# Optimization experiments

Hardware: AMD Instinct MI355X
Metric: run time of the kernel (lower is better)

## Reference

```python
import jax, jax.numpy as jnp
import numpy as np

B, S, D = 2, 2048, 2048
H, KVH, HD = 16, 4, 128
GROUPS = H // KVH
SCALE = HD ** -0.5


def rotate_half(x):
    half = x.shape[-1] // 2
    return jnp.concatenate((-x[..., half:], x[..., :half]), axis=-1)


def apply_rope(q, k, cos, sin):
    # q,k: [B,S,H,HD]; cos,sin: [S,HD//2] -> repeat_interleave(2) -> [S,HD]
    cos = jnp.repeat(cos, 2, axis=-1)[None, :, None, :]
    sin = jnp.repeat(sin, 2, axis=-1)[None, :, None, :]
    return q * cos + rotate_half(q) * sin, k * cos + rotate_half(k) * sin


def setup_inputs() -> dict:
    key = jax.random.key(0)
    ks = jax.random.split(key, 8)
    inp = {
        'x': jax.random.normal(ks[0], (B, S, D), dtype=jnp.float32),
        'cos': jnp.cos(jnp.arange(S, dtype=jnp.float32)[:, None] * (1.0 / (10000.0 ** (jnp.arange(HD // 2, dtype=jnp.float32) / (HD // 2))))[None, :].reshape(1, HD // 2)),
        'sin': None,
        'mask': jnp.tril(jnp.ones((S, S), dtype=bool))[None, None, :, :],
        'Wq': jax.random.normal(ks[1], (D, H * HD), dtype=jnp.float32) * (D ** -0.5),
        'Wk': jax.random.normal(ks[2], (D, KVH * HD), dtype=jnp.float32) * (D ** -0.5),
        'Wv': jax.random.normal(ks[3], (D, KVH * HD), dtype=jnp.float32) * (D ** -0.5),
        'Wo': jax.random.normal(ks[4], (H * HD, D), dtype=jnp.float32) * ((H * HD) ** -0.5),
    }
    inv_freq = 1.0 / (10000.0 ** (jnp.arange(0, HD // 2, dtype=jnp.float32) / (HD // 2)))
    freqs = jnp.arange(S, dtype=jnp.float32)[:, None] * inv_freq[None, :]  # [S, HD//2]
    inp['cos'] = jnp.cos(freqs)
    inp['sin'] = jnp.sin(freqs)
    return inp


def reference(x, cos, sin, mask, Wq, Wk, Wv, Wo):
    b, s, _ = x.shape
    q = (x @ Wq).reshape(b, s, H, HD)    # [B,S,H,HD]
    k = (x @ Wk).reshape(b, s, KVH, HD)  # [B,S,KVH,HD]
    v = (x @ Wv).reshape(b, s, KVH, HD)
    q, k = apply_rope(q, k, cos, sin)
    q = q.transpose(0, 2, 1, 3)  # [B,H,S,HD]
    k = k.transpose(0, 2, 1, 3)  # [B,KVH,S,HD]
    v = v.transpose(0, 2, 1, 3)
    k = jnp.repeat(k, GROUPS, axis=1)  # [B,H,S,HD]
    v = jnp.repeat(v, GROUPS, axis=1)
    scores = jnp.einsum('bhqd,bhkd->bhqk', q, k) * SCALE
    scores = jnp.where(mask, scores, -jnp.inf)
    attn = jax.nn.softmax(scores, axis=-1)
    out = jnp.einsum('bhqk,bhkd->bhqd', attn, v)
    out = out.transpose(0, 2, 1, 3).reshape(b, s, H * HD)
    return out @ Wo
```

## Files before the change

kernel.cpp:

```cpp
#include <hip/hip_runtime.h>
#include <hip/hip_bf16.h>
#include <cstdint>
#include <type_traits>

typedef __attribute__((ext_vector_type(8))) short short8;
typedef __attribute__((ext_vector_type(4))) float floatx4;

constexpr int S_LEN = 2048;
constexpr float ATTN_SCALE = 0.08838834764831845f;
constexpr float LOG2E = 1.4426950408889634f;
constexpr float CP = ATTN_SCALE * LOG2E;

__device__ __forceinline__ void gl_lds16(const void* gp, void* lp) {
  __builtin_amdgcn_global_load_lds(
      (__attribute__((address_space(1))) void*)(uintptr_t)gp,
      (__attribute__((address_space(3))) void*)lp,
      16, 0, 0);
}

__device__ __forceinline__ float rowmax16(float x) {
  union { float f; int i; } a, b;
  a.f = x;
  b.i = __builtin_amdgcn_update_dpp(0, a.i, 0x121, 0xF, 0xF, true);
  x = fmaxf(x, b.f); a.f = x;
  b.i = __builtin_amdgcn_update_dpp(0, a.i, 0x122, 0xF, 0xF, true);
  x = fmaxf(x, b.f); a.f = x;
  b.i = __builtin_amdgcn_update_dpp(0, a.i, 0x124, 0xF, 0xF, true);
  x = fmaxf(x, b.f); a.f = x;
  b.i = __builtin_amdgcn_update_dpp(0, a.i, 0x128, 0xF, 0xF, true);
  return fmaxf(x, b.f);
}

__global__ void cvt_bf16_kernel(const float* __restrict__ src,
                                __hip_bfloat16* __restrict__ dst, int n4) {
  int i = blockIdx.x * blockDim.x + threadIdx.x;
  if (i >= n4) return;
  float4 f = reinterpret_cast<const float4*>(src)[i];
  union { unsigned long long u64; __hip_bfloat16 h[4]; } u;
  u.h[0] = __float2bfloat16(f.x);
  u.h[1] = __float2bfloat16(f.y);
  u.h[2] = __float2bfloat16(f.z);
  u.h[3] = __float2bfloat16(f.w);
  reinterpret_cast<unsigned long long*>(dst)[i] = u.u64;
}

__global__ void transpose_bf16_kernel(const float* __restrict__ src,
                                      __hip_bfloat16* __restrict__ dst,
                                      int K, int N) {
  __shared__ float tile[32][33];
  int n0 = blockIdx.x * 32, k0 = blockIdx.y * 32;
  int tx = threadIdx.x, ty = threadIdx.y;
#pragma unroll
  for (int i = ty; i < 32; i += 8)
    tile[i][tx] = src[(size_t)(k0 + i) * N + n0 + tx];
  __syncthreads();
#pragma unroll
  for (int i = ty; i < 32; i += 8)
    dst[(size_t)(n0 + i) * K + k0 + tx] = __float2bfloat16(tile[tx][i]);
}

__global__ __launch_bounds__(256, 2) void qkv_gemm_kernel(
    const __hip_bfloat16* __restrict__ A,
    const __hip_bfloat16* __restrict__ Bt,
    __hip_bfloat16* __restrict__ qbuf,
    __hip_bfloat16* __restrict__ kbuf,
    __hip_bfloat16* __restrict__ vbuf) {
  constexpr int K = 2048;
  __shared__ __align__(16) __hip_bfloat16 lds[2 * 128 * 64];
  const int tid = threadIdx.x;
  const int wave = tid >> 6, lane = tid & 63;
  const int quad = lane >> 4, l15 = lane & 15;
  const int wm = wave >> 1, wn = wave & 1;
  const int m0 = blockIdx.y * 128, n0 = blockIdx.x * 128;

  floatx4 acc[4][4] = {};
  const __hip_bfloat16* Ab = A + (size_t)m0 * K;
  const __hip_bfloat16* Bb = Bt + (size_t)n0 * K;
  const int i0 = wave * 4;

  for (int k0 = 0; k0 < K; k0 += 64) {
#pragma unroll
    for (int j = 0; j < 4; ++j) {
      const int i = i0 + j;
      const int kchunk = i >> 1;
      const int row = ((i & 1) << 6) | lane;
      gl_lds16(Ab + (size_t)row * K + (k0 + kchunk * 8), &lds[i * 512]);
      gl_lds16(Bb + (size_t)row * K + (k0 + kchunk * 8), &lds[8192 + i * 512]);
    }
    __syncthreads();
#pragma unroll
    for (int kk = 0; kk < 2; ++kk) {
      short8 a[4], b[4];
#pragma unroll
      for (int mi = 0; mi < 4; ++mi)
        a[mi] = *(const short8*)&lds[((((kk << 2) | quad) * 128) + wm * 64 + mi * 16 + l15) * 8];
#pragma unroll
      for (int ni = 0; ni < 4; ++ni)
        b[ni] = *(const short8*)&lds[8192 + ((((kk << 2) | quad) * 128) + wn * 64 + ni * 16 + l15) * 8];
#pragma unroll
      for (int mi = 0; mi < 4; ++mi)
#pragma unroll
        for (int ni = 0; ni < 4; ++ni)
          acc[mi][ni] = __builtin_amdgcn_mfma_f32_16x16x32_bf16(a[mi], b[ni], acc[mi][ni], 0, 0, 0);
    }
    __syncthreads();
  }

  const int region = (n0 - 2048) >> 7;
  const int kvh = region & 3;
#pragma unroll
  for (int mi = 0; mi < 4; ++mi)
#pragma unroll
    for (int ni = 0; ni < 4; ++ni)
#pragma unroll
      for (int r = 0; r < 4; ++r) {
        int row = m0 + wm * 64 + mi * 16 + quad * 4 + r;
        int col = n0 + wn * 64 + ni * 16 + l15;
        __hip_bfloat16 val = __float2bfloat16(acc[mi][ni][r]);
        if (n0 < 2048) {
          qbuf[(size_t)row * 2048 + col] = val;
        } else {
          int d = wn * 64 + ni * 16 + l15;
          int s = row & (S_LEN - 1), bb = row >> 11;
          size_t tb = ((size_t)(bb * 4 + kvh) * 32 + (s >> 6)) * 8192;
          int kv = s & 63;
          if (region < 4)
            kbuf[tb + ((d >> 3) << 9) + (kv << 3) + (d & 7)] = val;
          else
            vbuf[tb + d * 64 + (kv ^ ((d & 7) << 3))] = val;
        }
      }
}

__global__ __launch_bounds__(256, 2) void gemm_bt_f32_kernel(
    const __hip_bfloat16* __restrict__ A,
    const __hip_bfloat16* __restrict__ Bt,
    float* __restrict__ C, int N, int K) {
  __shared__ __align__(16) __hip_bfloat16 lds[2 * 128 * 64];
  const int tid = threadIdx.x;
  const int wave = tid >> 6, lane = tid & 63;
  const int quad = lane >> 4, l15 = lane & 15;
  const int wm = wave >> 1, wn = wave & 1;
  const int m0 = blockIdx.y * 128, n0 = blockIdx.x * 128;

  floatx4 acc[4][4] = {};
  const __hip_bfloat16* Ab = A + (size_t)m0 * K;
  const __hip_bfloat16* Bb = Bt + (size_t)n0 * K;
  const int i0 = wave * 4;

  for (int k0 = 0; k0 < K; k0 += 64) {
#pragma unroll
    for (int j = 0; j < 4; ++j) {
      const int i = i0 + j;
      const int kchunk = i >> 1;
      const int row = ((i & 1) << 6) | lane;
      gl_lds16(Ab + (size_t)row * K + (k0 + kchunk * 8), &lds[i * 512]);
      gl_lds16(Bb + (size_t)row * K + (k0 + kchunk * 8), &lds[8192 + i * 512]);
    }
    __syncthreads();
#pragma unroll
    for (int kk = 0; kk < 2; ++kk) {
      short8 a[4], b[4];
#pragma unroll
      for (int mi = 0; mi < 4; ++mi)
        a[mi] = *(const short8*)&lds[((((kk << 2) | quad) * 128) + wm * 64 + mi * 16 + l15) * 8];
#pragma unroll
      for (int ni = 0; ni < 4; ++ni)
        b[ni] = *(const short8*)&lds[8192 + ((((kk << 2) | quad) * 128) + wn * 64 + ni * 16 + l15) * 8];
#pragma unroll
      for (int mi = 0; mi < 4; ++mi)
#pragma unroll
        for (int ni = 0; ni < 4; ++ni)
          acc[mi][ni] = __builtin_amdgcn_mfma_f32_16x16x32_bf16(a[mi], b[ni], acc[mi][ni], 0, 0, 0);
    }
    __syncthreads();
  }

#pragma unroll
  for (int mi = 0; mi < 4; ++mi)
#pragma unroll
    for (int ni = 0; ni < 4; ++ni)
#pragma unroll
      for (int r = 0; r < 4; ++r) {
        int row = m0 + wm * 64 + mi * 16 + quad * 4 + r;
        int col = n0 + wn * 64 + ni * 16 + l15;
        C[(size_t)row * N + col] = acc[mi][ni][r];
      }
}

__device__ __forceinline__ void rope8(short8 x0, short8 x1, const float* ca,
                                      const float* sa, const float* cb,
                                      const float* sb, short8& y0, short8& y1) {
#pragma unroll
  for (int e = 0; e < 8; ++e) {
    union { short s; __hip_bfloat16 h; } u0, u1, w0, w1;
    u0.s = x0[e]; u1.s = x1[e];
    float f0 = __bfloat162float(u0.h), f1 = __bfloat162float(u1.h);
    int j = e >> 1;
    w0.h = __float2bfloat16(f0 * ca[j] - f1 * sa[j]);
    w1.h = __float2bfloat16(f1 * cb[j] + f0 * sb[j]);
    y0[e] = w0.s; y1[e] = w1.s;
  }
}

__global__ void rope_q_kernel(__hip_bfloat16* __restrict__ qbuf,
                              const float* __restrict__ cosb,
                              const float* __restrict__ sinb) {
  int t = blockIdx.x * blockDim.x + threadIdx.x;
  int c8 = t & 7;
  int head = (t >> 3) & 15;
  int row = t >> 7;
  int s = row & (S_LEN - 1);
  size_t base = (size_t)row * 2048 + head * 128 + c8 * 8;
  short8 x0 = *(const short8*)(qbuf + base);
  short8 x1 = *(const short8*)(qbuf + base + 64);
  float ca[4], sa[4], cb[4], sb[4];
  *(float4*)ca = *(const float4*)&cosb[s * 64 + c8 * 4];
  *(float4*)sa = *(const float4*)&sinb[s * 64 + c8 * 4];
  *(float4*)cb = *(const float4*)&cosb[s * 64 + 32 + c8 * 4];
  *(float4*)sb = *(const float4*)&sinb[s * 64 + 32 + c8 * 4];
  short8 y0, y1;
  rope8(x0, x1, ca, sa, cb, sb, y0, y1);
  *(short8*)(qbuf + base) = y0;
  *(short8*)(qbuf + base + 64) = y1;
}

__global__ void rope_k_kernel(__hip_bfloat16* __restrict__ kbuf,
                              const float* __restrict__ cosb,
                              const float* __restrict__ sinb) {
  int t = blockIdx.x * blockDim.x + threadIdx.x;
  int c8 = t & 7;
  int kv = (t >> 3) & 63;
  int tile = t >> 9;
  int s = (tile & 31) * 64 + kv;
  size_t a0 = (size_t)tile * 8192 + c8 * 512 + kv * 8;
  short8 x0 = *(const short8*)(kbuf + a0);
  short8 x1 = *(const short8*)(kbuf + a0 + 4096);
  float ca[4], sa[4], cb[4], sb[4];
  *(float4*)ca = *(const float4*)&cosb[s * 64 + c8 * 4];
  *(float4*)sa = *(const float4*)&sinb[s * 64 + c8 * 4];
  *(float4*)cb = *(const float4*)&cosb[s * 64 + 32 + c8 * 4];
  *(float4*)sb = *(const float4*)&sinb[s * 64 + 32 + c8 * 4];
  short8 y0, y1;
  rope8(x0, x1, ca, sa, cb, sb, y0, y1);
  *(short8*)(kbuf + a0) = y0;
  *(short8*)(kbuf + a0 + 4096) = y1;
}

__global__ __launch_bounds__(256, 2) void attn_kernel(
    const __hip_bfloat16* __restrict__ qbuf,
    const __hip_bfloat16* __restrict__ kbuf,
    const __hip_bfloat16* __restrict__ vbuf,
    __hip_bfloat16* __restrict__ aout) {
  const int qt = (blockIdx.y & 16) ? blockIdx.x : (15 - blockIdx.x);
  const int bh = blockIdx.y;
  const int b = bh >> 4, h = bh & 15;
  const int kvh = h >> 2;

  __shared__ __align__(16) __hip_bfloat16 Kbuf[2][8192];
  __shared__ __align__(16) __hip_bfloat16 Vbuf[2][8192];
  __shared__ __align__(16) __hip_bfloat16 Plds[4 * 16 * 72];

  const int tid = threadIdx.x;
  const int wave = tid >> 6, lane = tid & 63;
  const int quad = lane >> 4, l15 = lane & 15;

  short8 qfrag[2][4];
#pragma unroll
  for (int rs = 0; rs < 2; ++rs)
#pragma unroll
    for (int kc = 0; kc < 4; ++kc)
      qfrag[rs][kc] = *(const short8*)(qbuf +
          (size_t)(b * S_LEN + qt * 128 + rs * 64 + wave * 16 + l15) * 2048 +
          h * 128 + kc * 32 + quad * 8);

  const __hip_bfloat16* ktiles = kbuf + (size_t)(b * 4 + kvh) * 32 * 8192;
  const __hip_bfloat16* vtiles = vbuf + (size_t)(b * 4 + kvh) * 32 * 8192;
  const int nt = 2 * qt + 2;

#pragma unroll
  for (int j = 0; j < 4; ++j) {
    int c = tid + 256 * j;
    gl_lds16(ktiles + c * 8, &Kbuf[0][c * 8]);
    gl_lds16(vtiles + c * 8, &Vbuf[0][c * 8]);
  }

  float m_r[2][4];
  floatx4 o[2][8] = {};
  floatx4 o_l[2] = {};
#pragma unroll
  for (int rs = 0; rs < 2; ++rs)
#pragma unroll
    for (int r = 0; r < 4; ++r) m_r[rs][r] = -1e30f;

  short8 onesb;
#pragma unroll
  for (int e = 0; e < 8; ++e) onesb[e] = (short)0x3F80;

  __hip_bfloat16* pw = &Plds[wave * 16 * 72];

  for (int kt = 0; kt < nt; ++kt) {
    const int cur = kt & 1;
    __syncthreads();

    if (kt + 1 < nt) {
      const __hip_bfloat16* kb = ktiles + (size_t)(kt + 1) * 8192;
      const __hip_bfloat16* vb = vtiles + (size_t)(kt + 1) * 8192;
#pragma unroll
      for (int j = 0; j < 4; ++j) {
        int c = tid + 256 * j;
        gl_lds16(kb + c * 8, &Kbuf[1 - cur][c * 8]);
        gl_lds16(vb + c * 8, &Vbuf[1 - cur][c * 8]);
      }
    }

    floatx4 sc[2][4] = {};
#pragma unroll
    for (int ni = 0; ni < 4; ++ni)
#pragma unroll
      for (int kc = 0; kc < 4; ++kc) {
        short8 bf = *(const short8*)&Kbuf[cur][((kc * 4 + quad) * 64 + ni * 16 + l15) * 8];
        sc[0][ni] = __builtin_amdgcn_mfma_f32_16x16x32_bf16(qfrag[0][kc], bf, sc[0][ni], 0, 0, 0);
        sc[1][ni] = __builtin_amdgcn_mfma_f32_16x16x32_bf16(qfrag[1][kc], bf, sc[1][ni], 0, 0, 0);
      }

#pragma unroll
    for (int rs = 0; rs < 2; ++rs) {
      const int qt64 = 2 * qt + rs;
      if (kt > qt64) continue;
      if (kt == qt64) {
        const int qrow = qt * 128 + rs * 64 + wave * 16 + quad * 4;
#pragma unroll
        for (int ni = 0; ni < 4; ++ni) {
          int kvcol = kt * 64 + ni * 16 + l15;
#pragma unroll
          for (int r = 0; r < 4; ++r)
            if (kvcol > qrow + r) sc[rs][ni][r] = -1e30f;
        }
      }

      float alpha[4];
#pragma unroll
      for (int r = 0; r < 4; ++r) {
        float v = fmaxf(fmaxf(sc[rs][0][r], sc[rs][1][r]),
                        fmaxf(sc[rs][2][r], sc[rs][3][r]));
        v = rowmax16(v);
        float mnew = fmaxf(m_r[rs][r], v);
        alpha[r] = exp2f((m_r[rs][r] - mnew) * CP);
        m_r[rs][r] = mnew;
        float mc = mnew * CP;
#pragma unroll
        for (int ni = 0; ni < 4; ++ni) {
          float p = exp2f(sc[rs][ni][r] * CP - mc);
          pw[(quad * 4 + r) * 72 + ni * 16 + l15] = __float2bfloat16(p);
        }
      }

#pragma unroll
      for (int nc = 0; nc < 8; ++nc)
#pragma unroll
        for (int r = 0; r < 4; ++r) o[rs][nc][r] *= alpha[r];
#pragma unroll
      for (int r = 0; r < 4; ++r) o_l[rs][r] *= alpha[r];

#pragma unroll
      for (int kk2 = 0; kk2 < 2; ++kk2) {
        short8 pa = *(const short8*)&pw[l15 * 72 + kk2 * 32 + quad * 8];
#pragma unroll
        for (int nc = 0; nc < 8; ++nc) {
          int d = nc * 16 + l15;
          int swcol = (kk2 * 32 + quad * 8) ^ ((d & 7) << 3);
          short8 vv = *(const short8*)&Vbuf[cur][d * 64 + swcol];
          o[rs][nc] = __builtin_amdgcn_mfma_f32_16x16x32_bf16(pa, vv, o[rs][nc], 0, 0, 0);
        }
        o_l[rs] = __builtin_amdgcn_mfma_f32_16x16x32_bf16(pa, onesb, o_l[rs], 0, 0, 0);
      }
    }
  }

#pragma unroll
  for (int rs = 0; rs < 2; ++rs) {
    float inv[4];
#pragma unroll
    for (int r = 0; r < 4; ++r) inv[r] = 1.0f / o_l[rs][r];
    const size_t orow0 = (size_t)(b * S_LEN + qt * 128 + rs * 64 + wave * 16 + quad * 4);
#pragma unroll
    for (int nc = 0; nc < 8; ++nc)
#pragma unroll
      for (int r = 0; r < 4; ++r)
        aout[(orow0 + r) * 2048 + h * 128 + nc * 16 + l15] =
            __float2bfloat16(o[rs][nc][r] * inv[r]);
  }
}

extern "C" void kernel_launch(void* const* d_in, const int* in_sizes, int n_in,
                              void* d_out, int out_size, void* d_ws, size_t ws_size,
                              hipStream_t stream) {
  const float* x    = (const float*)d_in[0];
  const float* cosb = (const float*)d_in[1];
  const float* sinb = (const float*)d_in[2];
  const float* Wq = (const float*)d_in[4];
  const float* Wk = (const float*)d_in[5];
  const float* Wv = (const float*)d_in[6];
  const float* Wo = (const float*)d_in[7];
  float* out = (float*)d_out;

  char* ws = (char*)d_ws;
  __hip_bfloat16* xb    = (__hip_bfloat16*)(ws);
  __hip_bfloat16* wqkvt = (__hip_bfloat16*)(ws + (16u << 20));
  __hip_bfloat16* wot   = (__hip_bfloat16*)(ws + (28u << 20));
  __hip_bfloat16* qbuf  = (__hip_bfloat16*)(ws + (36u << 20));
  __hip_bfloat16* kbuf  = (__hip_bfloat16*)(ws + (52u << 20));
  __hip_bfloat16* vbuf  = (__hip_bfloat16*)(ws + (56u << 20));
  __hip_bfloat16* aout  = (__hip_bfloat16*)(ws + (60u << 20));

  dim3 tb(32, 8);
  cvt_bf16_kernel<<<8192, 256, 0, stream>>>(x, xb, 2097152);
  transpose_bf16_kernel<<<dim3(64, 64), tb, 0, stream>>>(Wq, wqkvt, 2048, 2048);
  transpose_bf16_kernel<<<dim3(16, 64), tb, 0, stream>>>(Wk, wqkvt + 2048 * 2048, 2048, 512);
  transpose_bf16_kernel<<<dim3(16, 64), tb, 0, stream>>>(Wv, wqkvt + 2560 * 2048, 2048, 512);
  transpose_bf16_kernel<<<dim3(64, 64), tb, 0, stream>>>(Wo, wot, 2048, 2048);

  qkv_gemm_kernel<<<dim3(24, 32), 256, 0, stream>>>(xb, wqkvt, qbuf, kbuf, vbuf);
  rope_q_kernel<<<2048, 256, 0, stream>>>(qbuf, cosb, sinb);
  rope_k_kernel<<<512, 256, 0, stream>>>(kbuf, cosb, sinb);
  attn_kernel<<<dim3(16, 32), 256, 0, stream>>>(qbuf, kbuf, vbuf, aout);
  gemm_bt_f32_kernel<<<dim3(16, 32), 256, 0, stream>>>(aout, wot, out, 2048, 2048);
}
```

Measured before the change: 435.1 us.

## Merge prep and rope launches, shrink GEMM tiles to 64x128, batch attention PV MFMAs

Folds the x conversion and four weight transposes into one prep kernel, and merges the q and k rope kernels into one launch, cutting seven launches down to two. Both GEMMs move from 128x128 to 64x128 tiles with occupancy 4, doubling the block count to fill more CUs. The attention inner loop now loads both row-slices' P fragments first, then issues the PV MFMAs for both against each V fragment, so V is read from LDS once. In exchange the GEMMs get less reuse per block, and diagonal tiles now always go through masking.

```diff
diff --git a/kernel.cpp b/kernel.cpp
--- a/kernel.cpp
+++ b/kernel.cpp
@@ -31,90 +31,113 @@
   return fmaxf(x, b.f);
 }
 
-__global__ void cvt_bf16_kernel(const float* __restrict__ src,
-                                __hip_bfloat16* __restrict__ dst, int n4) {
-  int i = blockIdx.x * blockDim.x + threadIdx.x;
-  if (i >= n4) return;
-  float4 f = reinterpret_cast<const float4*>(src)[i];
-  union { unsigned long long u64; __hip_bfloat16 h[4]; } u;
-  u.h[0] = __float2bfloat16(f.x);
-  u.h[1] = __float2bfloat16(f.y);
-  u.h[2] = __float2bfloat16(f.z);
-  u.h[3] = __float2bfloat16(f.w);
-  reinterpret_cast<unsigned long long*>(dst)[i] = u.u64;
-}
-
-__global__ void transpose_bf16_kernel(const float* __restrict__ src,
-                                      __hip_bfloat16* __restrict__ dst,
-                                      int K, int N) {
-  __shared__ float tile[32][33];
-  int n0 = blockIdx.x * 32, k0 = blockIdx.y * 32;
-  int tx = threadIdx.x, ty = threadIdx.y;
+__device__ __forceinline__ void tr32(const float* __restrict__ src,
+                                     __hip_bfloat16* __restrict__ dst,
+                                     int blk, int nblk_x, int N, int tid,
+                                     float (*tile)[33]) {
+  int n0 = (blk % nblk_x) * 32, k0 = (blk / nblk_x) * 32;
+  int tx = tid & 31, ty = tid >> 5;
 #pragma unroll
   for (int i = ty; i < 32; i += 8)
     tile[i][tx] = src[(size_t)(k0 + i) * N + n0 + tx];
   __syncthreads();
 #pragma unroll
   for (int i = ty; i < 32; i += 8)
-    dst[(size_t)(n0 + i) * K + k0 + tx] = __float2bfloat16(tile[tx][i]);
-}
-
-__global__ __launch_bounds__(256, 2) void qkv_gemm_kernel(
+    dst[(size_t)(n0 + i) * 2048 + k0 + tx] = __float2bfloat16(tile[tx][i]);
+}
+
+__global__ void prep_kernel(const float* __restrict__ x,
+                            const float* __restrict__ Wq,
+                            const float* __restrict__ Wk,
+                            const float* __restrict__ Wv,
+                            const float* __restrict__ Wo,
+                            __hip_bfloat16* __restrict__ xb,
+                            __hip_bfloat16* __restrict__ wqkvt,
+                            __hip_bfloat16* __restrict__ wot) {
+  __shared__ float tile[32][33];
+  int bx = blockIdx.x, tid = threadIdx.x;
+  if (bx < 8192) {
+    int i = bx * 256 + tid;
+    float4 f = reinterpret_cast<const float4*>(x)[i];
+    union { unsigned long long u64; __hip_bfloat16 h[4]; } u;
+    u.h[0] = __float2bfloat16(f.x);
+    u.h[1] = __float2bfloat16(f.y);
+    u.h[2] = __float2bfloat16(f.z);
+    u.h[3] = __float2bfloat16(f.w);
+    reinterpret_cast<unsigned long long*>(xb)[i] = u.u64;
+  } else if (bx < 12288) {
+    tr32(Wq, wqkvt, bx - 8192, 64, 2048, tid, tile);
+  } else if (bx < 13312) {
+    tr32(Wk, wqkvt + 2048 * 2048, bx - 12288, 16, 512, tid, tile);
+  } else if (bx < 14336) {
+    tr32(Wv, wqkvt + 2560 * 2048, bx - 13312, 16, 512, tid, tile);
+  } else {
+    tr32(Wo, wot, bx - 14336, 64, 2048, tid, tile);
+  }
+}
+
+#define GEMM_STAGE(Ab, Bb, Alds, Blds, K, k0)                                   \
+  {                                                                             \
+    _Pragma("unroll") for (int j = 0; j < 6; ++j) {                             \
+      const int i = wave * 6 + j;                                               \
+      if (i < 8) {                                                              \
+        gl_lds16(Ab + (size_t)lane * (K) + (k0) + i * 8, &Alds[(i * 64 + lane) * 8]); \
+      } else {                                                                  \
+        const int ii = i - 8, kchunk = ii >> 1, row = ((ii & 1) << 6) | lane;   \
+        gl_lds16(Bb + (size_t)row * (K) + (k0) + kchunk * 8,                    \
+                 &Blds[(kchunk * 128 + row) * 8]);                              \
+      }                                                                         \
+    }                                                                           \
+  }
+
+#define GEMM_COMPUTE(Alds, Blds)                                                \
+  _Pragma("unroll") for (int kk = 0; kk < 2; ++kk) {                            \
+    short8 a[2], b[4];                                                          \
+    _Pragma("unroll") for (int mi = 0; mi < 2; ++mi)                            \
+      a[mi] = *(const short8*)&Alds[(((kk * 4 + quad) * 64) + wm * 32 + mi * 16 + l15) * 8]; \
+    _Pragma("unroll") for (int ni = 0; ni < 4; ++ni)                            \
+      b[ni] = *(const short8*)&Blds[(((kk * 4 + quad) * 128) + wn * 64 + ni * 16 + l15) * 8]; \
+    _Pragma("unroll") for (int mi = 0; mi < 2; ++mi)                            \
+      _Pragma("unroll") for (int ni = 0; ni < 4; ++ni)                          \
+        acc[mi][ni] = __builtin_amdgcn_mfma_f32_16x16x32_bf16(a[mi], b[ni], acc[mi][ni], 0, 0, 0); \
+  }
+
+__global__ __launch_bounds__(256, 4) void qkv_gemm_kernel(
     const __hip_bfloat16* __restrict__ A,
     const __hip_bfloat16* __restrict__ Bt,
     __hip_bfloat16* __restrict__ qbuf,
     __hip_bfloat16* __restrict__ kbuf,
     __hip_bfloat16* __restrict__ vbuf) {
   constexpr int K = 2048;
-  __shared__ __align__(16) __hip_bfloat16 lds[2 * 128 * 64];
+  __shared__ __align__(16) __hip_bfloat16 lds[4096 + 8192];
+  __hip_bfloat16* Alds = lds;
+  __hip_bfloat16* Blds = lds + 4096;
   const int tid = threadIdx.x;
   const int wave = tid >> 6, lane = tid & 63;
   const int quad = lane >> 4, l15 = lane & 15;
   const int wm = wave >> 1, wn = wave & 1;
-  const int m0 = blockIdx.y * 128, n0 = blockIdx.x * 128;
-
-  floatx4 acc[4][4] = {};
+  const int m0 = blockIdx.y * 64, n0 = blockIdx.x * 128;
+
+  floatx4 acc[2][4] = {};
   const __hip_bfloat16* Ab = A + (size_t)m0 * K;
   const __hip_bfloat16* Bb = Bt + (size_t)n0 * K;
-  const int i0 = wave * 4;
 
   for (int k0 = 0; k0 < K; k0 += 64) {
-#pragma unroll
-    for (int j = 0; j < 4; ++j) {
-      const int i = i0 + j;
-      const int kchunk = i >> 1;
-      const int row = ((i & 1) << 6) | lane;
-      gl_lds16(Ab + (size_t)row * K + (k0 + kchunk * 8), &lds[i * 512]);
-      gl_lds16(Bb + (size_t)row * K + (k0 + kchunk * 8), &lds[8192 + i * 512]);
-    }
+    GEMM_STAGE(Ab, Bb, Alds, Blds, K, k0)
     __syncthreads();
-#pragma unroll
-    for (int kk = 0; kk < 2; ++kk) {
-      short8 a[4], b[4];
-#pragma unroll
-      for (int mi = 0; mi < 4; ++mi)
-        a[mi] = *(const short8*)&lds[((((kk << 2) | quad) * 128) + wm * 64 + mi * 16 + l15) * 8];
-#pragma unroll
-      for (int ni = 0; ni < 4; ++ni)
-        b[ni] = *(const short8*)&lds[8192 + ((((kk << 2) | quad) * 128) + wn * 64 + ni * 16 + l15) * 8];
-#pragma unroll
-      for (int mi = 0; mi < 4; ++mi)
-#pragma unroll
-        for (int ni = 0; ni < 4; ++ni)
-          acc[mi][ni] = __builtin_amdgcn_mfma_f32_16x16x32_bf16(a[mi], b[ni], acc[mi][ni], 0, 0, 0);
-    }
+    GEMM_COMPUTE(Alds, Blds)
     __syncthreads();
   }
 
   const int region = (n0 - 2048) >> 7;
   const int kvh = region & 3;
 #pragma unroll
-  for (int mi = 0; mi < 4; ++mi)
+  for (int mi = 0; mi < 2; ++mi)
 #pragma unroll
     for (int ni = 0; ni < 4; ++ni)
 #pragma unroll
       for (int r = 0; r < 4; ++r) {
-        int row = m0 + wm * 64 + mi * 16 + quad * 4 + r;
+        int row = m0 + wm * 32 + mi * 16 + quad * 4 + r;
         int col = n0 + wn * 64 + ni * 16 + l15;
         __hip_bfloat16 val = __float2bfloat16(acc[mi][ni][r]);
         if (n0 < 2048) {
@@ -132,57 +155,37 @@
       }
 }
 
-__global__ __launch_bounds__(256, 2) void gemm_bt_f32_kernel(
+__global__ __launch_bounds__(256, 4) void gemm_bt_f32_kernel(
     const __hip_bfloat16* __restrict__ A,
     const __hip_bfloat16* __restrict__ Bt,
     float* __restrict__ C, int N, int K) {
-  __shared__ __align__(16) __hip_bfloat16 lds[2 * 128 * 64];
+  __shared__ __align__(16) __hip_bfloat16 lds[4096 + 8192];
+  __hip_bfloat16* Alds = lds;
+  __hip_bfloat16* Blds = lds + 4096;
   const int tid = threadIdx.x;
   const int wave = tid >> 6, lane = tid & 63;
   const int quad = lane >> 4, l15 = lane & 15;
   const int wm = wave >> 1, wn = wave & 1;
-  const int m0 = blockIdx.y * 128, n0 = blockIdx.x * 128;
-
-  floatx4 acc[4][4] = {};
+  const int m0 = blockIdx.y * 64, n0 = blockIdx.x * 128;
+
+  floatx4 acc[2][4] = {};
   const __hip_bfloat16* Ab = A + (size_t)m0 * K;
   const __hip_bfloat16* Bb = Bt + (size_t)n0 * K;
-  const int i0 = wave * 4;
 
   for (int k0 = 0; k0 < K; k0 += 64) {
-#pragma unroll
-    for (int j = 0; j < 4; ++j) {
-      const int i = i0 + j;
-      const int kchunk = i >> 1;
-      const int row = ((i & 1) << 6) | lane;
-      gl_lds16(Ab + (size_t)row * K + (k0 + kchunk * 8), &lds[i * 512]);
-      gl_lds16(Bb + (size_t)row * K + (k0 + kchunk * 8), &lds[8192 + i * 512]);
-    }
+    GEMM_STAGE(Ab, Bb, Alds, Blds, K, k0)
     __syncthreads();
-#pragma unroll
-    for (int kk = 0; kk < 2; ++kk) {
-      short8 a[4], b[4];
-#pragma unroll
-      for (int mi = 0; mi < 4; ++mi)
-        a[mi] = *(const short8*)&lds[((((kk << 2) | quad) * 128) + wm * 64 + mi * 16 + l15) * 8];
-#pragma unroll
-      for (int ni = 0; ni < 4; ++ni)
-        b[ni] = *(const short8*)&lds[8192 + ((((kk << 2) | quad) * 128) + wn * 64 + ni * 16 + l15) * 8];
-#pragma unroll
-      for (int mi = 0; mi < 4; ++mi)
-#pragma unroll
-        for (int ni = 0; ni < 4; ++ni)
-          acc[mi][ni] = __builtin_amdgcn_mfma_f32_16x16x32_bf16(a[mi], b[ni], acc[mi][ni], 0, 0, 0);
-    }
+    GEMM_COMPUTE(Alds, Blds)
     __syncthreads();
   }
 
 #pragma unroll
-  for (int mi = 0; mi < 4; ++mi)
+  for (int mi = 0; mi < 2; ++mi)
 #pragma unroll
     for (int ni = 0; ni < 4; ++ni)
 #pragma unroll
       for (int r = 0; r < 4; ++r) {
-        int row = m0 + wm * 64 + mi * 16 + quad * 4 + r;
+        int row = m0 + wm * 32 + mi * 16 + quad * 4 + r;
         int col = n0 + wn * 64 + ni * 16 + l15;
         C[(size_t)row * N + col] = acc[mi][ni][r];
       }
@@ -203,48 +206,47 @@
   }
 }
 
-__global__ void rope_q_kernel(__hip_bfloat16* __restrict__ qbuf,
-                              const float* __restrict__ cosb,
-                              const float* __restrict__ sinb) {
-  int t = blockIdx.x * blockDim.x + threadIdx.x;
-  int c8 = t & 7;
-  int head = (t >> 3) & 15;
-  int row = t >> 7;
-  int s = row & (S_LEN - 1);
-  size_t base = (size_t)row * 2048 + head * 128 + c8 * 8;
-  short8 x0 = *(const short8*)(qbuf + base);
-  short8 x1 = *(const short8*)(qbuf + base + 64);
+__global__ void rope_kernel(__hip_bfloat16* __restrict__ qbuf,
+                            __hip_bfloat16* __restrict__ kbuf,
+                            const float* __restrict__ cosb,
+                            const float* __restrict__ sinb) {
+  int bx = blockIdx.x, tid = threadIdx.x;
   float ca[4], sa[4], cb[4], sb[4];
-  *(float4*)ca = *(const float4*)&cosb[s * 64 + c8 * 4];
-  *(float4*)sa = *(const float4*)&sinb[s * 64 + c8 * 4];
-  *(float4*)cb = *(const float4*)&cosb[s * 64 + 32 + c8 * 4];
-  *(float4*)sb = *(const float4*)&sinb[s * 64 + 32 + c8 * 4];
-  short8 y0, y1;
-  rope8(x0, x1, ca, sa, cb, sb, y0, y1);
-  *(short8*)(qbuf + base) = y0;
-  *(short8*)(qbuf + base + 64) = y1;
-}
-
-__global__ void rope_k_kernel(__hip_bfloat16* __restrict__ kbuf,
-                              const float* __restrict__ cosb,
-                              const float* __restrict__ sinb) {
-  int t = blockIdx.x * blockDim.x + threadIdx.x;
-  int c8 = t & 7;
-  int kv = (t >> 3) & 63;
-  int tile = t >> 9;
-  int s = (tile & 31) * 64 + kv;
-  size_t a0 = (size_t)tile * 8192 + c8 * 512 + kv * 8;
-  short8 x0 = *(const short8*)(kbuf + a0);
-  short8 x1 = *(const short8*)(kbuf + a0 + 4096);
-  float ca[4], sa[4], cb[4], sb[4];
-  *(float4*)ca = *(const float4*)&cosb[s * 64 + c8 * 4];
-  *(float4*)sa = *(const float4*)&sinb[s * 64 + c8 * 4];
-  *(float4*)cb = *(const float4*)&cosb[s * 64 + 32 + c8 * 4];
-  *(float4*)sb = *(const float4*)&sinb[s * 64 + 32 + c8 * 4];
-  short8 y0, y1;
-  rope8(x0, x1, ca, sa, cb, sb, y0, y1);
-  *(short8*)(kbuf + a0) = y0;
-  *(short8*)(kbuf + a0 + 4096) = y1;
+  if (bx < 2048) {
+    int t = bx * 256 + tid;
+    int c8 = t & 7;
+    int head = (t >> 3) & 15;
+    int row = t >> 7;
+    int s = row & (S_LEN - 1);
+    size_t base = (size_t)row * 2048 + head * 128 + c8 * 8;
+    short8 x0 = *(const short8*)(qbuf + base);
+    short8 x1 = *(const short8*)(qbuf + base + 64);
+    *(float4*)ca = *(const float4*)&cosb[s * 64 + c8 * 4];
+    *(float4*)sa = *(const float4*)&sinb[s * 64 + c8 * 4];
+    *(float4*)cb = *(const float4*)&cosb[s * 64 + 32 + c8 * 4];
+    *(float4*)sb = *(const float4*)&sinb[s * 64 + 32 + c8 * 4];
+    short8 y0, y1;
+    rope8(x0, x1, ca, sa, cb, sb, y0, y1);
+    *(short8*)(qbuf + base) = y0;
+    *(short8*)(qbuf + base + 64) = y1;
+  } else {
+    int t = (bx - 2048) * 256 + tid;
+    int c8 = t & 7;
+    int kv = (t >> 3) & 63;
+    int tile = t >> 9;
+    int s = (tile & 31) * 64 + kv;
+    size_t a0 = (size_t)tile * 8192 + c8 * 512 + kv * 8;
+    short8 x0 = *(const short8*)(kbuf + a0);
+    short8 x1 = *(const short8*)(kbuf + a0 + 4096);
+    *(float4*)ca = *(const float4*)&cosb[s * 64 + c8 * 4];
+    *(float4*)sa = *(const float4*)&sinb[s * 64 + c8 * 4];
+    *(float4*)cb = *(const float4*)&cosb[s * 64 + 32 + c8 * 4];
+    *(float4*)sb = *(const float4*)&sinb[s * 64 + 32 + c8 * 4];
+    short8 y0, y1;
+    rope8(x0, x1, ca, sa, cb, sb, y0, y1);
+    *(short8*)(kbuf + a0) = y0;
+    *(short8*)(kbuf + a0 + 4096) = y1;
+  }
 }
 
 __global__ __launch_bounds__(256, 2) void attn_kernel(
@@ -324,11 +326,11 @@
         sc[1][ni] = __builtin_amdgcn_mfma_f32_16x16x32_bf16(qfrag[1][kc], bf, sc[1][ni], 0, 0, 0);
       }
 
+    short8 pa[2][2];
 #pragma unroll
     for (int rs = 0; rs < 2; ++rs) {
       const int qt64 = 2 * qt + rs;
-      if (kt > qt64) continue;
-      if (kt == qt64) {
+      if (kt >= qt64) {
         const int qrow = qt * 128 + rs * 64 + wave * 16 + quad * 4;
 #pragma unroll
         for (int ni = 0; ni < 4; ++ni) {
@@ -357,24 +359,29 @@
       }
 
 #pragma unroll
+      for (int kk2 = 0; kk2 < 2; ++kk2)
+        pa[rs][kk2] = *(const short8*)&pw[l15 * 72 + kk2 * 32 + quad * 8];
+
+#pragma unroll
       for (int nc = 0; nc < 8; ++nc)
 #pragma unroll
         for (int r = 0; r < 4; ++r) o[rs][nc][r] *= alpha[r];
 #pragma unroll
       for (int r = 0; r < 4; ++r) o_l[rs][r] *= alpha[r];
-
-#pragma unroll
-      for (int kk2 = 0; kk2 < 2; ++kk2) {
-        short8 pa = *(const short8*)&pw[l15 * 72 + kk2 * 32 + quad * 8];
-#pragma unroll
-        for (int nc = 0; nc < 8; ++nc) {
-          int d = nc * 16 + l15;
-          int swcol = (kk2 * 32 + quad * 8) ^ ((d & 7) << 3);
-          short8 vv = *(const short8*)&Vbuf[cur][d * 64 + swcol];
-          o[rs][nc] = __builtin_amdgcn_mfma_f32_16x16x32_bf16(pa, vv, o[rs][nc], 0, 0, 0);
-        }
-        o_l[rs] = __builtin_amdgcn_mfma_f32_16x16x32_bf16(pa, onesb, o_l[rs], 0, 0, 0);
-      }
+    }
+
+#pragma unroll
+    for (int kk2 = 0; kk2 < 2; ++kk2) {
+#pragma unroll
+      for (int nc = 0; nc < 8; ++nc) {
+        int d = nc * 16 + l15;
+        int swcol = (kk2 * 32 + quad * 8) ^ ((d & 7) << 3);
+        short8 vv = *(const short8*)&Vbuf[cur][d * 64 + swcol];
+        o[0][nc] = __builtin_amdgcn_mfma_f32_16x16x32_bf16(pa[0][kk2], vv, o[0][nc], 0, 0, 0);
+        o[1][nc] = __builtin_amdgcn_mfma_f32_16x16x32_bf16(pa[1][kk2], vv, o[1][nc], 0, 0, 0);
+      }
+      o_l[0] = __builtin_amdgcn_mfma_f32_16x16x32_bf16(pa[0][kk2], onesb, o_l[0], 0, 0, 0);
+      o_l[1] = __builtin_amdgcn_mfma_f32_16x16x32_bf16(pa[1][kk2], onesb, o_l[1], 0, 0, 0);
     }
   }
 
@@ -414,16 +421,9 @@
   __hip_bfloat16* vbuf  = (__hip_bfloat16*)(ws + (56u << 20));
   __hip_bfloat16* aout  = (__hip_bfloat16*)(ws + (60u << 20));
 
-  dim3 tb(32, 8);
-  cvt_bf16_kernel<<<8192, 256, 0, stream>>>(x, xb, 2097152);
-  transpose_bf16_kernel<<<dim3(64, 64), tb, 0, stream>>>(Wq, wqkvt, 2048, 2048);
-  transpose_bf16_kernel<<<dim3(16, 64), tb, 0, stream>>>(Wk, wqkvt + 2048 * 2048, 2048, 512);
-  transpose_bf16_kernel<<<dim3(16, 64), tb, 0, stream>>>(Wv, wqkvt + 2560 * 2048, 2048, 512);
-  transpose_bf16_kernel<<<dim3(64, 64), tb, 0, stream>>>(Wo, wot, 2048, 2048);
-
-  qkv_gemm_kernel<<<dim3(24, 32), 256, 0, stream>>>(xb, wqkvt, qbuf, kbuf, vbuf);
-  rope_q_kernel<<<2048, 256, 0, stream>>>(qbuf, cosb, sinb);
-  rope_k_kernel<<<512, 256, 0, stream>>>(kbuf, cosb, sinb);
+  prep_kernel<<<18432, 256, 0, stream>>>(x, Wq, Wk, Wv, Wo, xb, wqkvt, wot);
+  qkv_gemm_kernel<<<dim3(24, 64), 256, 0, stream>>>(xb, wqkvt, qbuf, kbuf, vbuf);
+  rope_kernel<<<2560, 256, 0, stream>>>(qbuf, kbuf, cosb, sinb);
   attn_kernel<<<dim3(16, 32), 256, 0, stream>>>(qbuf, kbuf, vbuf, aout);
-  gemm_bt_f32_kernel<<<dim3(16, 32), 256, 0, stream>>>(aout, wot, out, 2048, 2048);
-}
+  gemm_bt_f32_kernel<<<dim3(16, 64), 256, 0, stream>>>(aout, wot, out, 2048, 2048);
+}
```

Result: slower. 489.2 us (+12.4%).

## Fuse prep kernels, fold RoPE into QKV GEMM epilogue, batch attention PV MFMAs

Applied to the files above, without the earlier changes.

The five conversion and transpose launches are merged into one prep kernel. The separate RoPE passes over Q and K are removed by staging GEMM tiles through LDS and applying RoPE in the QKV GEMM epilogue, which also writes vectorized, layout-transformed K and V stores. In attention, the PV MFMA loop now runs once per kv tile for both row sets, sharing each V fragment load. The diagonal-tile condition changes from skip-or-mask to mask-always, so fully masked tiles now do computation. The goal is fewer launches, less global traffic and fewer V reads from LDS, at the cost of extra LDS round-trips in the epilogue.

```diff
diff --git a/kernel.cpp b/kernel.cpp
--- a/kernel.cpp
+++ b/kernel.cpp
@@ -31,32 +31,64 @@
   return fmaxf(x, b.f);
 }
 
-__global__ void cvt_bf16_kernel(const float* __restrict__ src,
-                                __hip_bfloat16* __restrict__ dst, int n4) {
-  int i = blockIdx.x * blockDim.x + threadIdx.x;
-  if (i >= n4) return;
-  float4 f = reinterpret_cast<const float4*>(src)[i];
-  union { unsigned long long u64; __hip_bfloat16 h[4]; } u;
-  u.h[0] = __float2bfloat16(f.x);
-  u.h[1] = __float2bfloat16(f.y);
-  u.h[2] = __float2bfloat16(f.z);
-  u.h[3] = __float2bfloat16(f.w);
-  reinterpret_cast<unsigned long long*>(dst)[i] = u.u64;
-}
-
-__global__ void transpose_bf16_kernel(const float* __restrict__ src,
-                                      __hip_bfloat16* __restrict__ dst,
-                                      int K, int N) {
-  __shared__ float tile[32][33];
-  int n0 = blockIdx.x * 32, k0 = blockIdx.y * 32;
-  int tx = threadIdx.x, ty = threadIdx.y;
+__device__ __forceinline__ void rope8(short8 x0, short8 x1, const float* ca,
+                                      const float* sa, const float* cb,
+                                      const float* sb, short8& y0, short8& y1) {
+#pragma unroll
+  for (int e = 0; e < 8; ++e) {
+    union { short s; __hip_bfloat16 h; } u0, u1, w0, w1;
+    u0.s = x0[e]; u1.s = x1[e];
+    float f0 = __bfloat162float(u0.h), f1 = __bfloat162float(u1.h);
+    int j = e >> 1;
+    w0.h = __float2bfloat16(f0 * ca[j] - f1 * sa[j]);
+    w1.h = __float2bfloat16(f1 * cb[j] + f0 * sb[j]);
+    y0[e] = w0.s; y1[e] = w1.s;
+  }
+}
+
+__device__ __forceinline__ void tr32(const float* __restrict__ src,
+                                     __hip_bfloat16* __restrict__ dst,
+                                     int blk, int nblk_x, int N, int tid,
+                                     float (*tile)[33]) {
+  int n0 = (blk % nblk_x) * 32, k0 = (blk / nblk_x) * 32;
+  int tx = tid & 31, ty = tid >> 5;
 #pragma unroll
   for (int i = ty; i < 32; i += 8)
     tile[i][tx] = src[(size_t)(k0 + i) * N + n0 + tx];
   __syncthreads();
 #pragma unroll
   for (int i = ty; i < 32; i += 8)
-    dst[(size_t)(n0 + i) * K + k0 + tx] = __float2bfloat16(tile[tx][i]);
+    dst[(size_t)(n0 + i) * 2048 + k0 + tx] = __float2bfloat16(tile[tx][i]);
+}
+
+__global__ void prep_kernel(const float* __restrict__ x,
+                            const float* __restrict__ Wq,
+                            const float* __restrict__ Wk,
+                            const float* __restrict__ Wv,
+                            const float* __restrict__ Wo,
+                            __hip_bfloat16* __restrict__ xb,
+                            __hip_bfloat16* __restrict__ wqkvt,
+                            __hip_bfloat16* __restrict__ wot) {
+  __shared__ float tile[32][33];
+  int bx = blockIdx.x, tid = threadIdx.x;
+  if (bx < 8192) {
+    int i = bx * 256 + tid;
+    float4 f = reinterpret_cast<const float4*>(x)[i];
+    union { unsigned long long u64; __hip_bfloat16 h[4]; } u;
+    u.h[0] = __float2bfloat16(f.x);
+    u.h[1] = __float2bfloat16(f.y);
+    u.h[2] = __float2bfloat16(f.z);
+    u.h[3] = __float2bfloat16(f.w);
+    reinterpret_cast<unsigned long long*>(xb)[i] = u.u64;
+  } else if (bx < 12288) {
+    tr32(Wq, wqkvt, bx - 8192, 64, 2048, tid, tile);
+  } else if (bx < 13312) {
+    tr32(Wk, wqkvt + 2048 * 2048, bx - 12288, 16, 512, tid, tile);
+  } else if (bx < 14336) {
+    tr32(Wv, wqkvt + 2560 * 2048, bx - 13312, 16, 512, tid, tile);
+  } else {
+    tr32(Wo, wot, bx - 14336, 64, 2048, tid, tile);
+  }
 }
 
 __global__ __launch_bounds__(256, 2) void qkv_gemm_kernel(
@@ -64,7 +96,9 @@
     const __hip_bfloat16* __restrict__ Bt,
     __hip_bfloat16* __restrict__ qbuf,
     __hip_bfloat16* __restrict__ kbuf,
-    __hip_bfloat16* __restrict__ vbuf) {
+    __hip_bfloat16* __restrict__ vbuf,
+    const float* __restrict__ cosb,
+    const float* __restrict__ sinb) {
   constexpr int K = 2048;
   __shared__ __align__(16) __hip_bfloat16 lds[2 * 128 * 64];
   const int tid = threadIdx.x;
@@ -106,30 +140,80 @@
     __syncthreads();
   }
 
-  const int region = (n0 - 2048) >> 7;
-  const int kvh = region & 3;
+  const bool isv = (n0 >= 2560);
+  short* lds2 = (short*)lds;
 #pragma unroll
   for (int mi = 0; mi < 4; ++mi)
 #pragma unroll
     for (int ni = 0; ni < 4; ++ni)
 #pragma unroll
       for (int r = 0; r < 4; ++r) {
-        int row = m0 + wm * 64 + mi * 16 + quad * 4 + r;
-        int col = n0 + wn * 64 + ni * 16 + l15;
-        __hip_bfloat16 val = __float2bfloat16(acc[mi][ni][r]);
-        if (n0 < 2048) {
-          qbuf[(size_t)row * 2048 + col] = val;
-        } else {
-          int d = wn * 64 + ni * 16 + l15;
-          int s = row & (S_LEN - 1), bb = row >> 11;
-          size_t tb = ((size_t)(bb * 4 + kvh) * 32 + (s >> 6)) * 8192;
-          int kv = s & 63;
-          if (region < 4)
-            kbuf[tb + ((d >> 3) << 9) + (kv << 3) + (d & 7)] = val;
-          else
-            vbuf[tb + d * 64 + (kv ^ ((d & 7) << 3))] = val;
-        }
-      }
+        int row = wm * 64 + mi * 16 + quad * 4 + r;
+        int col = wn * 64 + ni * 16 + l15;
+        union { short s; __hip_bfloat16 h; } u;
+        u.h = __float2bfloat16(acc[mi][ni][r]);
+        if (isv) lds2[col * 128 + row] = u.s;
+        else     lds2[row * 128 + col] = u.s;
+      }
+  __syncthreads();
+
+  const int c8 = tid & 7, d0 = c8 * 8;
+  if (n0 < 2048) {
+#pragma unroll
+    for (int j = 0; j < 4; ++j) {
+      int rr = (tid >> 3) + 32 * j;
+      int rowg = m0 + rr;
+      int s = rowg & (S_LEN - 1);
+      float ca[4], sa[4], cb[4], sb[4];
+      *(float4*)ca = *(const float4*)&cosb[s * 64 + c8 * 4];
+      *(float4*)sa = *(const float4*)&sinb[s * 64 + c8 * 4];
+      *(float4*)cb = *(const float4*)&cosb[s * 64 + 32 + c8 * 4];
+      *(float4*)sb = *(const float4*)&sinb[s * 64 + 32 + c8 * 4];
+      short8 x0 = *(const short8*)&lds2[rr * 128 + d0];
+      short8 x1 = *(const short8*)&lds2[rr * 128 + 64 + d0];
+      short8 y0, y1;
+      rope8(x0, x1, ca, sa, cb, sb, y0, y1);
+      *(short8*)(qbuf + (size_t)rowg * 2048 + n0 + d0) = y0;
+      *(short8*)(qbuf + (size_t)rowg * 2048 + n0 + 64 + d0) = y1;
+    }
+  } else if (!isv) {
+    const int kvh = (n0 - 2048) >> 7;
+#pragma unroll
+    for (int j = 0; j < 4; ++j) {
+      int rr = (tid >> 3) + 32 * j;
+      int rowg = m0 + rr;
+      int s = rowg & (S_LEN - 1), bb = rowg >> 11;
+      int kv = s & 63;
+      size_t tb = ((size_t)(bb * 4 + kvh) * 32 + (s >> 6)) * 8192;
+      float ca[4], sa[4], cb[4], sb[4];
+      *(float4*)ca = *(const float4*)&cosb[s * 64 + c8 * 4];
+      *(float4*)sa = *(const float4*)&sinb[s * 64 + c8 * 4];
+      *(float4*)cb = *(const float4*)&cosb[s * 64 + 32 + c8 * 4];
+      *(float4*)sb = *(const float4*)&sinb[s * 64 + 32 + c8 * 4];
+      short8 x0 = *(const short8*)&lds2[rr * 128 + d0];
+      short8 x1 = *(const short8*)&lds2[rr * 128 + 64 + d0];
+      short8 y0, y1;
+      rope8(x0, x1, ca, sa, cb, sb, y0, y1);
+      *(short8*)(kbuf + tb + (size_t)c8 * 512 + kv * 8) = y0;
+      *(short8*)(kbuf + tb + (size_t)(8 + c8) * 512 + kv * 8) = y1;
+    }
+  } else {
+    const int kvh = (n0 - 2560) >> 7;
+    const int bb = m0 >> 11;
+    const int kt0 = (m0 & (S_LEN - 1)) >> 6;
+    const int kv0 = c8 * 8;
+#pragma unroll
+    for (int j = 0; j < 4; ++j) {
+      int d = (tid >> 3) + 32 * j;
+      int cxor = (d & 7) << 3;
+#pragma unroll
+      for (int half = 0; half < 2; ++half) {
+        short8 vv = *(const short8*)&lds2[d * 128 + half * 64 + kv0];
+        size_t tb = ((size_t)(bb * 4 + kvh) * 32 + kt0 + half) * 8192;
+        *(short8*)(vbuf + tb + d * 64 + (kv0 ^ cxor)) = vv;
+      }
+    }
+  }
 }
 
 __global__ __launch_bounds__(256, 2) void gemm_bt_f32_kernel(
@@ -188,65 +272,6 @@
       }
 }
 
-__device__ __forceinline__ void rope8(short8 x0, short8 x1, const float* ca,
-                                      const float* sa, const float* cb,
-                                      const float* sb, short8& y0, short8& y1) {
-#pragma unroll
-  for (int e = 0; e < 8; ++e) {
-    union { short s; __hip_bfloat16 h; } u0, u1, w0, w1;
-    u0.s = x0[e]; u1.s = x1[e];
-    float f0 = __bfloat162float(u0.h), f1 = __bfloat162float(u1.h);
-    int j = e >> 1;
-    w0.h = __float2bfloat16(f0 * ca[j] - f1 * sa[j]);
-    w1.h = __float2bfloat16(f1 * cb[j] + f0 * sb[j]);
-    y0[e] = w0.s; y1[e] = w1.s;
-  }
-}
-
-__global__ void rope_q_kernel(__hip_bfloat16* __restrict__ qbuf,
-                              const float* __restrict__ cosb,
-                              const float* __restrict__ sinb) {
-  int t = blockIdx.x * blockDim.x + threadIdx.x;
-  int c8 = t & 7;
-  int head = (t >> 3) & 15;
-  int row = t >> 7;
-  int s = row & (S_LEN - 1);
-  size_t base = (size_t)row * 2048 + head * 128 + c8 * 8;
-  short8 x0 = *(const short8*)(qbuf + base);
-  short8 x1 = *(const short8*)(qbuf + base + 64);
-  float ca[4], sa[4], cb[4], sb[4];
-  *(float4*)ca = *(const float4*)&cosb[s * 64 + c8 * 4];
-  *(float4*)sa = *(const float4*)&sinb[s * 64 + c8 * 4];
-  *(float4*)cb = *(const float4*)&cosb[s * 64 + 32 + c8 * 4];
-  *(float4*)sb = *(const float4*)&sinb[s * 64 + 32 + c8 * 4];
-  short8 y0, y1;
-  rope8(x0, x1, ca, sa, cb, sb, y0, y1);
-  *(short8*)(qbuf + base) = y0;
-  *(short8*)(qbuf + base + 64) = y1;
-}
-
-__global__ void rope_k_kernel(__hip_bfloat16* __restrict__ kbuf,
-                              const float* __restrict__ cosb,
-                              const float* __restrict__ sinb) {
-  int t = blockIdx.x * blockDim.x + threadIdx.x;
-  int c8 = t & 7;
-  int kv = (t >> 3) & 63;
-  int tile = t >> 9;
-  int s = (tile & 31) * 64 + kv;
-  size_t a0 = (size_t)tile * 8192 + c8 * 512 + kv * 8;
-  short8 x0 = *(const short8*)(kbuf + a0);
-  short8 x1 = *(const short8*)(kbuf + a0 + 4096);
-  float ca[4], sa[4], cb[4], sb[4];
-  *(float4*)ca = *(const float4*)&cosb[s * 64 + c8 * 4];
-  *(float4*)sa = *(const float4*)&sinb[s * 64 + c8 * 4];
-  *(float4*)cb = *(const float4*)&cosb[s * 64 + 32 + c8 * 4];
-  *(float4*)sb = *(const float4*)&sinb[s * 64 + 32 + c8 * 4];
-  short8 y0, y1;
-  rope8(x0, x1, ca, sa, cb, sb, y0, y1);
-  *(short8*)(kbuf + a0) = y0;
-  *(short8*)(kbuf + a0 + 4096) = y1;
-}
-
 __global__ __launch_bounds__(256, 2) void attn_kernel(
     const __hip_bfloat16* __restrict__ qbuf,
     const __hip_bfloat16* __restrict__ kbuf,
@@ -324,11 +349,11 @@
         sc[1][ni] = __builtin_amdgcn_mfma_f32_16x16x32_bf16(qfrag[1][kc], bf, sc[1][ni], 0, 0, 0);
       }
 
+    short8 pa[2][2];
 #pragma unroll
     for (int rs = 0; rs < 2; ++rs) {
       const int qt64 = 2 * qt + rs;
-      if (kt > qt64) continue;
-      if (kt == qt64) {
+      if (kt >= qt64) {
         const int qrow = qt * 128 + rs * 64 + wave * 16 + quad * 4;
 #pragma unroll
         for (int ni = 0; ni < 4; ++ni) {
@@ -357,24 +382,29 @@
       }
 
 #pragma unroll
+      for (int kk2 = 0; kk2 < 2; ++kk2)
+        pa[rs][kk2] = *(const short8*)&pw[l15 * 72 + kk2 * 32 + quad * 8];
+
+#pragma unroll
       for (int nc = 0; nc < 8; ++nc)
 #pragma unroll
         for (int r = 0; r < 4; ++r) o[rs][nc][r] *= alpha[r];
 #pragma unroll
       for (int r = 0; r < 4; ++r) o_l[rs][r] *= alpha[r];
-
-#pragma unroll
-      for (int kk2 = 0; kk2 < 2; ++kk2) {
-        short8 pa = *(const short8*)&pw[l15 * 72 + kk2 * 32 + quad * 8];
-#pragma unroll
-        for (int nc = 0; nc < 8; ++nc) {
-          int d = nc * 16 + l15;
-          int swcol = (kk2 * 32 + quad * 8) ^ ((d & 7) << 3);
-          short8 vv = *(const short8*)&Vbuf[cur][d * 64 + swcol];
-          o[rs][nc] = __builtin_amdgcn_mfma_f32_16x16x32_bf16(pa, vv, o[rs][nc], 0, 0, 0);
-        }
-        o_l[rs] = __builtin_amdgcn_mfma_f32_16x16x32_bf16(pa, onesb, o_l[rs], 0, 0, 0);
-      }
+    }
+
+#pragma unroll
+    for (int kk2 = 0; kk2 < 2; ++kk2) {
+#pragma unroll
+      for (int nc = 0; nc < 8; ++nc) {
+        int d = nc * 16 + l15;
+        int swcol = (kk2 * 32 + quad * 8) ^ ((d & 7) << 3);
+        short8 vv = *(const short8*)&Vbuf[cur][d * 64 + swcol];
+        o[0][nc] = __builtin_amdgcn_mfma_f32_16x16x32_bf16(pa[0][kk2], vv, o[0][nc], 0, 0, 0);
+        o[1][nc] = __builtin_amdgcn_mfma_f32_16x16x32_bf16(pa[1][kk2], vv, o[1][nc], 0, 0, 0);
+      }
+      o_l[0] = __builtin_amdgcn_mfma_f32_16x16x32_bf16(pa[0][kk2], onesb, o_l[0], 0, 0, 0);
+      o_l[1] = __builtin_amdgcn_mfma_f32_16x16x32_bf16(pa[1][kk2], onesb, o_l[1], 0, 0, 0);
     }
   }
 
@@ -414,16 +444,8 @@
   __hip_bfloat16* vbuf  = (__hip_bfloat16*)(ws + (56u << 20));
   __hip_bfloat16* aout  = (__hip_bfloat16*)(ws + (60u << 20));
 
-  dim3 tb(32, 8);
-  cvt_bf16_kernel<<<8192, 256, 0, stream>>>(x, xb, 2097152);
-  transpose_bf16_kernel<<<dim3(64, 64), tb, 0, stream>>>(Wq, wqkvt, 2048, 2048);
-  transpose_bf16_kernel<<<dim3(16, 64), tb, 0, stream>>>(Wk, wqkvt + 2048 * 2048, 2048, 512);
-  transpose_bf16_kernel<<<dim3(16, 64), tb, 0, stream>>>(Wv, wqkvt + 2560 * 2048, 2048, 512);
-  transpose_bf16_kernel<<<dim3(64, 64), tb, 0, stream>>>(Wo, wot, 2048, 2048);
-
-  qkv_gemm_kernel<<<dim3(24, 32), 256, 0, stream>>>(xb, wqkvt, qbuf, kbuf, vbuf);
-  rope_q_kernel<<<2048, 256, 0, stream>>>(qbuf, cosb, sinb);
-  rope_k_kernel<<<512, 256, 0, stream>>>(kbuf, cosb, sinb);
+  prep_kernel<<<18432, 256, 0, stream>>>(x, Wq, Wk, Wv, Wo, xb, wqkvt, wot);
+  qkv_gemm_kernel<<<dim3(24, 32), 256, 0, stream>>>(xb, wqkvt, qbuf, kbuf, vbuf, cosb, sinb);
   attn_kernel<<<dim3(16, 32), 256, 0, stream>>>(qbuf, kbuf, vbuf, aout);
   gemm_bt_f32_kernel<<<dim3(16, 32), 256, 0, stream>>>(aout, wot, out, 2048, 2048);
 }
```

Measured after the change: 413.0 us. -5.1%, faster.
